# Kernel optimization log

Measured on AMD Instinct MI355X. Metric: run time of the kernel, lower is better.

The kernel has to match this reference:

```python
import jax, jax.numpy as jnp
import numpy as np

EMBED_DIM = 2048
N_HEADS = 16
D_HEAD = EMBED_DIM // N_HEADS


def setup_inputs() -> dict:
    key = jax.random.key(0)
    kx, kq, kk, kv = jax.random.split(key, 4)
    B, N, D = 4, 2048, EMBED_DIM
    x = jax.random.normal(kx, (B, N, D), dtype=jnp.float32)
    Wq = jax.random.normal(kq, (D, D), dtype=jnp.float32) * 0.02
    Wk = jax.random.normal(kk, (D, D), dtype=jnp.float32) * 0.02
    Wv = jax.random.normal(kv, (D, D), dtype=jnp.float32) * 0.02
    return {"x": x, "Wq": Wq, "Wk": Wk, "Wv": Wv}


def reference(x, Wq, Wk, Wv):
    # x: [B, N, D]; weights applied as x @ W (matching torch.matmul in source)
    B, N, D = x.shape
    H, d = N_HEADS, D_HEAD
    # [B, N, D] -> [B, H, N, d]
    Q = (x @ Wq).reshape(B, N, H, d).transpose(0, 2, 1, 3)
    K = (x @ Wk).reshape(B, N, H, d).transpose(0, 2, 1, 3)
    V = (x @ Wv).reshape(B, N, H, d).transpose(0, 2, 1, 3)
    scale = 1.0 / jnp.sqrt(jnp.asarray(d, dtype=x.dtype))
    # non-causal SDPA (torch default: no mask, scale = 1/sqrt(d_head))
    scores = jnp.einsum('bhqd,bhkd->bhqk', Q, K) * scale  # [B,H,N,N]
    attn = jax.nn.softmax(scores, axis=-1)
    out = jnp.einsum('bhqk,bhkd->bhqd', attn, V)  # [B,H,N,d]
    return out
```

## Files before the change

kernel.cpp:

```cpp
#include <hip/hip_runtime.h>
#include <hip/hip_bf16.h>

#define B 4
#define N 2048
#define D 2048
#define H 16
#define DH 128
#define NT 32

typedef unsigned short u16;
typedef __attribute__((ext_vector_type(8))) short short8;
typedef __attribute__((ext_vector_type(4))) float floatx4;

__device__ __forceinline__ u16 f2b(float f) {
    union { __hip_bfloat16 h; u16 u; } cv;
    cv.h = __float2bfloat16(f);
    return cv.u;
}

__device__ __forceinline__ floatx4 mfma16(short8 a, short8 b, floatx4 c) {
    return __builtin_amdgcn_mfma_f32_16x16x32_bf16(a, b, c, 0, 0, 0);
}

#if __has_builtin(__builtin_amdgcn_exp2f)
#define EXP2(x) __builtin_amdgcn_exp2f(x)
#else
#define EXP2(x) exp2f(x)
#endif

__device__ __forceinline__ void async16(const void* g, void* l) {
    __builtin_amdgcn_global_load_lds(
        (const __attribute__((address_space(1))) unsigned int*)g,
        (__attribute__((address_space(3))) unsigned int*)l, 16, 0, 0);
}

__global__ __launch_bounds__(256) void cvt_x(const float* __restrict__ x,
                                             u16* __restrict__ xb) {
    size_t i = ((size_t)blockIdx.x * 256 + threadIdx.x) * 8;
    float4 v0 = *(const float4*)&x[i];
    float4 v1 = *(const float4*)&x[i + 4];
    union { u16 u[8]; uint4 s; } pk;
    pk.u[0] = f2b(v0.x); pk.u[1] = f2b(v0.y); pk.u[2] = f2b(v0.z); pk.u[3] = f2b(v0.w);
    pk.u[4] = f2b(v1.x); pk.u[5] = f2b(v1.y); pk.u[6] = f2b(v1.z); pk.u[7] = f2b(v1.w);
    *(uint4*)&xb[i] = pk.s;
}

__global__ __launch_bounds__(256) void cvt_w_t(const float* __restrict__ Wq,
                                               const float* __restrict__ Wk,
                                               const float* __restrict__ Wv,
                                               u16* __restrict__ wt) {
    __shared__ float tile[64][65];
    const int z = blockIdx.z;
    const float* W = (z == 0) ? Wq : (z == 1) ? Wk : Wv;
    const float scl = (z == 0) ? 0.12751743342f : 1.0f;
    const int k0 = blockIdx.x * 64, n0 = blockIdx.y * 64;
    const int tr = threadIdx.x >> 4, tc = threadIdx.x & 15;
#pragma unroll
    for (int i = 0; i < 4; i++) {
        int kk = tr + 16 * i;
        float4 vv = *(const float4*)&W[(size_t)(k0 + kk) * D + n0 + tc * 4];
        tile[kk][tc * 4 + 0] = vv.x; tile[kk][tc * 4 + 1] = vv.y;
        tile[kk][tc * 4 + 2] = vv.z; tile[kk][tc * 4 + 3] = vv.w;
    }
    __syncthreads();
#pragma unroll
    for (int i = 0; i < 4; i++) {
        int nn = tr + 16 * i;
        union { u16 u[4]; ushort4 s; } pk;
#pragma unroll
        for (int j = 0; j < 4; j++) pk.u[j] = f2b(tile[tc * 4 + j][nn] * scl);
        *(ushort4*)&wt[(size_t)z * D * D + (size_t)(n0 + nn) * D + k0 + tc * 4] = pk.s;
    }
}

__global__ __launch_bounds__(256) void qkv_gemm(const u16* __restrict__ xb,
                                                const u16* __restrict__ wt,
                                                u16* __restrict__ qo,
                                                u16* __restrict__ ko,
                                                u16* __restrict__ vo) {
    __shared__ u16 As[128][32];
    __shared__ u16 Bs[128][32];
    const int nt = blockIdx.x;
    const int z = nt >> 4, ntile = nt & 15;
    const int mt = blockIdx.y;
    const int t = threadIdx.x, lane = t & 63, w = t >> 6;
    const int wr = w >> 1, wc = w & 1;
    const int half = lane >> 4, lr = lane & 15;
    const size_t abase = (size_t)mt * 128 * D;
    const size_t bbase = (size_t)z * D * D + (size_t)ntile * 128 * D;

    floatx4 acc[4][4];
#pragma unroll
    for (int i = 0; i < 4; i++)
#pragma unroll
        for (int j = 0; j < 4; j++) acc[i][j] = (floatx4){0.f, 0.f, 0.f, 0.f};

    for (int kt = 0; kt < D / 32; kt++) {
        __syncthreads();
#pragma unroll
        for (int c = 0; c < 2; c++) {
            int grp = 2 * w + c;
            int row = 16 * grp + (lane >> 2);
            int g = lane & 3;
            async16(&xb[abase + (size_t)row * D + kt * 32 + g * 8],
                    (char*)As + grp * 1024);
            async16(&wt[bbase + (size_t)row * D + kt * 32 + g * 8],
                    (char*)Bs + grp * 1024);
        }
        __syncthreads();
        short8 a[4];
#pragma unroll
        for (int rt = 0; rt < 4; rt++)
            a[rt] = *(const short8*)&As[64 * wr + 16 * rt + lr][half * 8];
#pragma unroll
        for (int ct = 0; ct < 4; ct++) {
            short8 b = *(const short8*)&Bs[64 * wc + 16 * ct + lr][half * 8];
#pragma unroll
            for (int rt = 0; rt < 4; rt++)
                acc[rt][ct] = mfma16(a[rt], b, acc[rt][ct]);
        }
    }

    u16* dst = (z == 0) ? qo : (z == 1) ? ko : vo;
#pragma unroll
    for (int rt = 0; rt < 4; rt++)
#pragma unroll
        for (int ct = 0; ct < 4; ct++)
#pragma unroll
            for (int r = 0; r < 4; r++) {
                int row = mt * 128 + 64 * wr + 16 * rt + 4 * half + r;
                int col = 64 * wc + 16 * ct + lr;
                int b_ = row >> 11, n_ = row & (N - 1);
                dst[((size_t)(b_ * H + ntile) * N + n_) * DH + col] = f2b(acc[rt][ct][r]);
            }
}

__global__ __launch_bounds__(256) void transpose_v(const u16* __restrict__ v,
                                                   u16* __restrict__ vt) {
    __shared__ u16 tile[64][72];
    const int bh = blockIdx.z;
    const int n0 = blockIdx.x * 64, d0 = blockIdx.y * 64;
    const int t = threadIdx.x;
#pragma unroll
    for (int i = 0; i < 2; i++) {
        int gid = t + 256 * i;
        int nl = gid >> 3, g = gid & 7;
        *(uint4*)&tile[nl][g * 8] =
            *(const uint4*)&v[((size_t)bh * N + n0 + nl) * DH + d0 + g * 8];
    }
    __syncthreads();
#pragma unroll
    for (int i = 0; i < 2; i++) {
        int gid = t + 256 * i;
        int dl = gid >> 3, gn = gid & 7;
        union { u16 u[8]; uint4 s; } pk;
#pragma unroll
        for (int j = 0; j < 8; j++) {
            int kp = gn * 8 + j;
            int src = 32 * (kp >> 5) + 16 * (kp & 1) + ((kp >> 1) & 15);
            pk.u[j] = tile[src][dl];
        }
        *(uint4*)&vt[((size_t)bh * DH + d0 + dl) * N + n0 + gn * 8] = pk.s;
    }
}

#define FMAX2 17.312340491f
__global__ __launch_bounds__(256, 2) void attn_kernel(const u16* __restrict__ q,
                                                      const u16* __restrict__ k,
                                                      const u16* __restrict__ vt,
                                                      float* __restrict__ out) {
    __shared__ u16 Ks[2][64][128];
    __shared__ u16 Vts[2][128][64];
    __shared__ u16 Ps[128][64];

    const int beta = blockIdx.x;
    const int bh = (beta & 7) + 8 * (beta >> 7);
    const int qt = (beta >> 3) & 15;
    const int t = threadIdx.x;
    const int w = t >> 6, lane = t & 63;
    const int half = lane >> 4, lr = lane & 15;
    const int a = w & 1, b = w >> 1;

    const size_t qbase = ((size_t)bh * N + (size_t)qt * 128) * DH;
    short8 af[4][4];
#pragma unroll
    for (int rt = 0; rt < 4; rt++)
#pragma unroll
        for (int ks = 0; ks < 4; ks++)
            af[rt][ks] = *(const short8*)&q[qbase + (size_t)(64 * b + 16 * rt + lr) * DH
                                            + ks * 32 + half * 8];

    float lrow[4][4];
    floatx4 o[4][4];
#pragma unroll
    for (int rt = 0; rt < 4; rt++)
#pragma unroll
        for (int r = 0; r < 4; r++) lrow[rt][r] = 0.f;
#pragma unroll
    for (int rt = 0; rt < 4; rt++)
#pragma unroll
        for (int ct = 0; ct < 4; ct++) o[rt][ct] = (floatx4){0.f, 0.f, 0.f, 0.f};

    const size_t kbase = (size_t)bh * N * DH;
    const size_t vtbase = (size_t)bh * DH * N;
    const u16* kp[4];
    const u16* vp[4];
#pragma unroll
    for (int c = 0; c < 4; c++) {
        int grp = 4 * w + c;
        int krow = 4 * grp + (lane >> 4);
        int kg = (lane & 15) ^ (krow & 15);
        kp[c] = &k[kbase + (size_t)krow * DH + kg * 8];
        int vrow = 8 * grp + (lane >> 3);
        int vg = (lane & 7) ^ (vrow & 7);
        vp[c] = &vt[vtbase + (size_t)vrow * N + vg * 8];
    }

#pragma unroll
    for (int c = 0; c < 4; c++) {
        async16(kp[c], (char*)&Ks[0][0][0] + (4 * w + c) * 1024);
        async16(vp[c], (char*)&Vts[0][0][0] + (4 * w + c) * 1024);
    }

    for (int kt = 0; kt < NT; kt++) {
        const int cur = kt & 1;
        __syncthreads();

        floatx4 sf[4][2];
#pragma unroll
        for (int ct = 0; ct < 2; ct++) {
            short8 bf[4];
#pragma unroll
            for (int ks = 0; ks < 4; ks++) {
                int gs = (4 * ks + half) ^ lr;
                bf[ks] = *(const short8*)&Ks[cur][32 * a + 16 * ct + lr][gs * 8];
            }
#pragma unroll
            for (int rt = 0; rt < 4; rt++) {
                floatx4 s = (floatx4){0.f, 0.f, 0.f, 0.f};
#pragma unroll
                for (int ks = 0; ks < 4; ks++) s = mfma16(af[rt][ks], bf[ks], s);
                sf[rt][ct] = s;
            }
        }

#pragma unroll
        for (int rt = 0; rt < 4; rt++)
#pragma unroll
            for (int r = 0; r < 4; r++) {
                int row = 64 * b + 16 * rt + 4 * half + r;
                float p0 = EXP2(sf[rt][0][r] - FMAX2);
                float p1 = EXP2(sf[rt][1][r] - FMAX2);
                lrow[rt][r] += p0 + p1;
                unsigned int pw = (unsigned int)f2b(p0) | ((unsigned int)f2b(p1) << 16);
                int u = (16 * a + lr) ^ ((row & 7) << 2);
                *(unsigned int*)&Ps[row][u * 2] = pw;
            }

        __syncthreads();

        if (kt + 1 < NT) {
            const int nb = cur ^ 1;
#pragma unroll
            for (int c = 0; c < 4; c++) {
                async16(kp[c] + (size_t)(kt + 1) * 64 * DH,
                        (char*)&Ks[nb][0][0] + (4 * w + c) * 1024);
                async16(vp[c] + (size_t)(kt + 1) * 64,
                        (char*)&Vts[nb][0][0] + (4 * w + c) * 1024);
            }
        }

#pragma unroll
        for (int ks = 0; ks < 2; ks++) {
            short8 a2[4];
#pragma unroll
            for (int rt = 0; rt < 4; rt++) {
                int g = (4 * ks + half) ^ (lr & 7);
                a2[rt] = *(const short8*)&Ps[64 * b + 16 * rt + lr][g * 8];
            }
#pragma unroll
            for (int ct = 0; ct < 4; ct++) {
                int dd = 64 * a + 16 * ct + lr;
                int gv = (4 * ks + half) ^ (lr & 7);
                short8 bv = *(const short8*)&Vts[cur][dd][gv * 8];
#pragma unroll
                for (int rt = 0; rt < 4; rt++)
                    o[rt][ct] = mfma16(a2[rt], bv, o[rt][ct]);
            }
        }
    }

    __syncthreads();
    float* Ls = (float*)&Ps[0][0];
#pragma unroll
    for (int rt = 0; rt < 4; rt++)
#pragma unroll
        for (int r = 0; r < 4; r++) {
            float s = lrow[rt][r];
            s += __shfl_xor(s, 1);
            s += __shfl_xor(s, 2);
            s += __shfl_xor(s, 4);
            s += __shfl_xor(s, 8);
            if (lr == 0) Ls[a * 128 + (64 * b + 16 * rt + 4 * half + r)] = s;
        }
    __syncthreads();
    const size_t obase = ((size_t)bh * N + (size_t)qt * 128) * DH;
#pragma unroll
    for (int rt = 0; rt < 4; rt++)
#pragma unroll
        for (int r = 0; r < 4; r++) {
            int row = 64 * b + 16 * rt + 4 * half + r;
            float inv = 1.f / (Ls[row] + Ls[128 + row]);
#pragma unroll
            for (int ct = 0; ct < 4; ct++)
                out[obase + (size_t)row * DH + 64 * a + 16 * ct + lr] = o[rt][ct][r] * inv;
        }
}

extern "C" void kernel_launch(void* const* d_in, const int* in_sizes, int n_in,
                              void* d_out, int out_size, void* d_ws, size_t ws_size,
                              hipStream_t stream) {
    const float* x  = (const float*)d_in[0];
    const float* Wq = (const float*)d_in[1];
    const float* Wk = (const float*)d_in[2];
    const float* Wv = (const float*)d_in[3];
    float* out = (float*)d_out;
    char* ws = (char*)d_ws;

    u16* xb = (u16*)(ws);
    u16* wt = (u16*)(ws + 33554432);
    u16* qb = (u16*)(ws + 58720256);
    u16* kb = (u16*)(ws + 92274688);
    u16* vb = (u16*)(ws + 125829120);
    u16* vtb = (u16*)(ws);

    cvt_x<<<dim3(8192), dim3(256), 0, stream>>>(x, xb);
    cvt_w_t<<<dim3(32, 32, 3), dim3(256), 0, stream>>>(Wq, Wk, Wv, wt);
    qkv_gemm<<<dim3(48, 64), dim3(256), 0, stream>>>(xb, wt, qb, kb, vb);
    transpose_v<<<dim3(32, 2, 64), dim3(256), 0, stream>>>(vb, vtb);
    attn_kernel<<<dim3(1024), dim3(256), 0, stream>>>(qb, kb, vtb, out);
}
```

Baseline: 534.1 us.

## Rewrite QKV GEMM with 256x256 tiles, double-buffered async loads and swizzled LDS

Replaces the 128x128, K=32 QKV projection GEMM with a 512-thread kernel that computes 256x256 output tiles using K=64 steps. Global-to-LDS async copies are double-buffered and interleaved with four MFMA phases per step, separated by explicit barriers and waitcnts, with raised wave priority during the MFMA phases. LDS rows use an XOR swizzle to avoid bank conflicts, and the block index is remapped for L2 locality. The larger tiles cut global traffic per flop but raise register pressure and depend on getting the fine-grained barrier and waitcnt choreography right.

New measurement: 499.2 us. 6.5% less time.

```diff
diff --git a/kernel.cpp b/kernel.cpp
--- a/kernel.cpp
+++ b/kernel.cpp
@@ -73,66 +73,175 @@
     }
 }
 
-__global__ __launch_bounds__(256) void qkv_gemm(const u16* __restrict__ xb,
-                                                const u16* __restrict__ wt,
-                                                u16* __restrict__ qo,
-                                                u16* __restrict__ ko,
-                                                u16* __restrict__ vo) {
-    __shared__ u16 As[128][32];
-    __shared__ u16 Bs[128][32];
-    const int nt = blockIdx.x;
-    const int z = nt >> 4, ntile = nt & 15;
-    const int mt = blockIdx.y;
+#define KT 32
+__global__ __launch_bounds__(512, 2) void qkv_gemm(const u16* __restrict__ xb,
+                                                   const u16* __restrict__ wt,
+                                                   u16* __restrict__ qo,
+                                                   u16* __restrict__ ko,
+                                                   u16* __restrict__ vo) {
+    __shared__ u16 lds[2][2][2][128 * 64];
+
+    const int bid = blockIdx.x;
+    const int swz = (bid & 7) * 96 + (bid >> 3);
+    const int tm = swz & 31;
+    const int tn = swz >> 5;
+
     const int t = threadIdx.x, lane = t & 63, w = t >> 6;
-    const int wr = w >> 1, wc = w & 1;
-    const int half = lane >> 4, lr = lane & 15;
-    const size_t abase = (size_t)mt * 128 * D;
-    const size_t bbase = (size_t)z * D * D + (size_t)ntile * 128 * D;
-
-    floatx4 acc[4][4];
-#pragma unroll
-    for (int i = 0; i < 4; i++)
+    const int wr = w >> 2, wc = w & 3;
+    const int q4 = lane >> 4, lr = lane & 15;
+
+    const int m0 = tm * 256;
+    const int n0 = tn * 256;
+
+    unsigned aoff[2][2], boff[2][2];
+#pragma unroll
+    for (int i = 0; i < 2; i++) {
+        const int off = i * 8192 + w * 1024 + lane * 16;
+        const int row = off >> 7;
+        const int s = (off >> 4) & 7;
+        const int col = ((s ^ (row & 7))) * 8;
+#pragma unroll
+        for (int h = 0; h < 2; h++) {
+            aoff[h][i] = (unsigned)((m0 + h * 128 + row) * D + col);
+            boff[h][i] = (unsigned)((n0 + h * 128 + row) * D + col);
+        }
+    }
+
+#define STAGE_A(buf, h, j) {                                                        \
+    async16(xb + aoff[h][0] + (unsigned)(j) * 64, (char*)&lds[buf][0][h][0] + w * 1024);        \
+    async16(xb + aoff[h][1] + (unsigned)(j) * 64, (char*)&lds[buf][0][h][0] + 8192 + w * 1024); }
+#define STAGE_B(buf, h, j) {                                                        \
+    async16(wt + boff[h][0] + (unsigned)(j) * 64, (char*)&lds[buf][1][h][0] + w * 1024);        \
+    async16(wt + boff[h][1] + (unsigned)(j) * 64, (char*)&lds[buf][1][h][0] + 8192 + w * 1024); }
+#define BAR() __builtin_amdgcn_s_barrier()
+#define LGKM0() asm volatile("s_waitcnt lgkmcnt(0)" ::: "memory")
+
+    floatx4 acc[8][4];
+#pragma unroll
+    for (int i = 0; i < 8; i++)
 #pragma unroll
         for (int j = 0; j < 4; j++) acc[i][j] = (floatx4){0.f, 0.f, 0.f, 0.f};
 
-    for (int kt = 0; kt < D / 32; kt++) {
-        __syncthreads();
-#pragma unroll
-        for (int c = 0; c < 2; c++) {
-            int grp = 2 * w + c;
-            int row = 16 * grp + (lane >> 2);
-            int g = lane & 3;
-            async16(&xb[abase + (size_t)row * D + kt * 32 + g * 8],
-                    (char*)As + grp * 1024);
-            async16(&wt[bbase + (size_t)row * D + kt * 32 + g * 8],
-                    (char*)Bs + grp * 1024);
-        }
-        __syncthreads();
-        short8 a[4];
-#pragma unroll
-        for (int rt = 0; rt < 4; rt++)
-            a[rt] = *(const short8*)&As[64 * wr + 16 * rt + lr][half * 8];
-#pragma unroll
-        for (int ct = 0; ct < 4; ct++) {
-            short8 b = *(const short8*)&Bs[64 * wc + 16 * ct + lr][half * 8];
-#pragma unroll
-            for (int rt = 0; rt < 4; rt++)
-                acc[rt][ct] = mfma16(a[rt], b, acc[rt][ct]);
-        }
-    }
-
+    STAGE_A(0, 0, 0); STAGE_A(0, 1, 0);
+    STAGE_B(0, 0, 0); STAGE_B(0, 1, 0);
+    STAGE_A(1, 0, 1); STAGE_A(1, 1, 1);
+    asm volatile("s_waitcnt vmcnt(4)" ::: "memory");
+    BAR();
+
+    for (int g = 0; g < KT; g++) {
+        const int cur = g & 1, nxt = cur ^ 1;
+        short8 a0[4][2], a1[4][2], b0[2][2], b1[2][2];
+
+#pragma unroll
+        for (int mf = 0; mf < 4; mf++) {
+            const int hrow = mf * 16 + lr;
+            const int sw = hrow & 7;
+#pragma unroll
+            for (int ks = 0; ks < 2; ks++)
+                a0[mf][ks] = *(const short8*)&lds[cur][0][wr][hrow * 64 + ((ks * 4 + q4) ^ sw) * 8];
+        }
+#pragma unroll
+        for (int nf = 0; nf < 2; nf++) {
+            const int hrow = (wc & 1) * 64 + nf * 16 + lr;
+            const int sw = hrow & 7;
+#pragma unroll
+            for (int ks = 0; ks < 2; ks++)
+                b0[nf][ks] = *(const short8*)&lds[cur][1][wc >> 1][hrow * 64 + ((ks * 4 + q4) ^ sw) * 8];
+        }
+        if (g + 1 < KT) STAGE_B(nxt, 0, g + 1);
+        BAR();
+        LGKM0();
+        __builtin_amdgcn_s_setprio(1);
+#pragma unroll
+        for (int nf = 0; nf < 2; nf++)
+#pragma unroll
+            for (int mf = 0; mf < 4; mf++)
+#pragma unroll
+                for (int ks = 0; ks < 2; ks++)
+                    acc[mf][nf] = mfma16(a0[mf][ks], b0[nf][ks], acc[mf][nf]);
+        __builtin_amdgcn_s_setprio(0);
+        BAR();
+
+#pragma unroll
+        for (int mf = 0; mf < 4; mf++) {
+            const int hrow = 64 + mf * 16 + lr;
+            const int sw = hrow & 7;
+#pragma unroll
+            for (int ks = 0; ks < 2; ks++)
+                a1[mf][ks] = *(const short8*)&lds[cur][0][wr][hrow * 64 + ((ks * 4 + q4) ^ sw) * 8];
+        }
+        if (g + 1 < KT) STAGE_B(nxt, 1, g + 1);
+        BAR();
+        LGKM0();
+        __builtin_amdgcn_s_setprio(1);
+#pragma unroll
+        for (int nf = 0; nf < 2; nf++)
+#pragma unroll
+            for (int mf = 0; mf < 4; mf++)
+#pragma unroll
+                for (int ks = 0; ks < 2; ks++)
+                    acc[4 + mf][nf] = mfma16(a1[mf][ks], b0[nf][ks], acc[4 + mf][nf]);
+        __builtin_amdgcn_s_setprio(0);
+        BAR();
+
+#pragma unroll
+        for (int nf = 0; nf < 2; nf++) {
+            const int hrow = (wc & 1) * 64 + (2 + nf) * 16 + lr;
+            const int sw = hrow & 7;
+#pragma unroll
+            for (int ks = 0; ks < 2; ks++)
+                b1[nf][ks] = *(const short8*)&lds[cur][1][wc >> 1][hrow * 64 + ((ks * 4 + q4) ^ sw) * 8];
+        }
+        if (g + 2 < KT) STAGE_A(cur, 0, g + 2);
+        BAR();
+        LGKM0();
+        __builtin_amdgcn_s_setprio(1);
+#pragma unroll
+        for (int nf = 0; nf < 2; nf++)
+#pragma unroll
+            for (int mf = 0; mf < 4; mf++)
+#pragma unroll
+                for (int ks = 0; ks < 2; ks++)
+                    acc[4 + mf][2 + nf] = mfma16(a1[mf][ks], b1[nf][ks], acc[4 + mf][2 + nf]);
+        __builtin_amdgcn_s_setprio(0);
+        BAR();
+
+        if (g + 2 < KT) STAGE_A(cur, 1, g + 2);
+        BAR();
+        __builtin_amdgcn_s_setprio(1);
+#pragma unroll
+        for (int nf = 0; nf < 2; nf++)
+#pragma unroll
+            for (int mf = 0; mf < 4; mf++)
+#pragma unroll
+                for (int ks = 0; ks < 2; ks++)
+                    acc[mf][2 + nf] = mfma16(a0[mf][ks], b1[nf][ks], acc[mf][2 + nf]);
+        __builtin_amdgcn_s_setprio(0);
+        if (g == KT - 2) { asm volatile("s_waitcnt vmcnt(0)" ::: "memory"); }
+        else if (g < KT - 2) { asm volatile("s_waitcnt vmcnt(4)" ::: "memory"); }
+        BAR();
+    }
+
+    const int z = tn >> 3;
     u16* dst = (z == 0) ? qo : (z == 1) ? ko : vo;
-#pragma unroll
-    for (int rt = 0; rt < 4; rt++)
-#pragma unroll
-        for (int ct = 0; ct < 4; ct++)
+    const int c2b = (tn & 7) * 256 + wc * 64;
+    const int grb = tm * 256 + wr * 128;
+#pragma unroll
+    for (int mf = 0; mf < 8; mf++)
+#pragma unroll
+        for (int nf = 0; nf < 4; nf++)
 #pragma unroll
             for (int r = 0; r < 4; r++) {
-                int row = mt * 128 + 64 * wr + 16 * rt + 4 * half + r;
-                int col = 64 * wc + 16 * ct + lr;
-                int b_ = row >> 11, n_ = row & (N - 1);
-                dst[((size_t)(b_ * H + ntile) * N + n_) * DH + col] = f2b(acc[rt][ct][r]);
-            }
+                int gr = grb + mf * 16 + q4 * 4 + r;
+                int c2 = c2b + nf * 16 + lr;
+                int b_ = gr >> 11, n_ = gr & (N - 1);
+                int head = c2 >> 7, dcol = c2 & 127;
+                dst[((size_t)(b_ * H + head) * N + n_) * DH + dcol] = f2b(acc[mf][nf][r]);
+            }
+#undef STAGE_A
+#undef STAGE_B
+#undef BAR
+#undef LGKM0
 }
 
 __global__ __launch_bounds__(256) void transpose_v(const u16* __restrict__ v,
@@ -336,7 +445,7 @@
 
     cvt_x<<<dim3(8192), dim3(256), 0, stream>>>(x, xb);
     cvt_w_t<<<dim3(32, 32, 3), dim3(256), 0, stream>>>(Wq, Wk, Wv, wt);
-    qkv_gemm<<<dim3(48, 64), dim3(256), 0, stream>>>(xb, wt, qb, kb, vb);
+    qkv_gemm<<<dim3(768), dim3(512), 0, stream>>>(xb, wt, qb, kb, vb);
     transpose_v<<<dim3(32, 2, 64), dim3(256), 0, stream>>>(vb, vtb);
     attn_kernel<<<dim3(1024), dim3(256), 0, stream>>>(qb, kb, vtb, out);
 }
```
